# Performance work log

Measured on AMD Instinct MI355X. Metric: run time of the kernel, lower is better.

Reference implementation:

```python
import jax, jax.numpy as jnp
import numpy as np

N_EXPERTS = 16
IN_DIM = 1024
OUT_DIM = 1024
BATCH = 4096

def setup_inputs() -> dict:
    key = jax.random.key(0)
    k1, k2, k3, k4 = jax.random.split(key, 4)
    x = jax.random.normal(k1, (BATCH, IN_DIM), dtype=jnp.float32)
    comp_weight = jax.random.uniform(k2, (BATCH, N_EXPERTS), dtype=jnp.float32)
    # torch.rand init (uniform [0,1)) per original module
    weight = jax.random.uniform(k3, (N_EXPERTS, IN_DIM, OUT_DIM), dtype=jnp.float32)
    bias = jax.random.uniform(k4, (N_EXPERTS, OUT_DIM), dtype=jnp.float32)
    return {"x": x, "comp_weight": comp_weight, "weight": weight, "bias": bias}

def reference(x, comp_weight, weight, bias):
    # z[n,b,o] = x[b,i] @ weight[n,i,o] + bias[n,o]   (baddbmm)
    z = jnp.einsum('bi,nio->nbo', x, weight) + bias[:, None, :]
    # out[b,o] = sum_n comp_weight[b,n] * z[n,b,o]    (bmm combine)
    out = jnp.einsum('bn,nbo->bo', comp_weight, z)
    return jax.nn.relu(out)
```

## Files before the change

### kernel.cpp

```cpp
#include <hip/hip_runtime.h>
#include <hip/hip_bf16.h>
#include <cstdint>

#define BATCH   4096
#define IN_DIM  1024
#define OUT_DIM 1024
#define NEXP    16

typedef __bf16 bf16;
typedef __attribute__((ext_vector_type(8))) __bf16 bf16x8;
typedef __attribute__((ext_vector_type(4))) float  f32x4;

#define AS1 __attribute__((address_space(1)))
#define AS3 __attribute__((address_space(3)))

__device__ __forceinline__ void gld_lds16(const bf16* g, bf16* l) {
    __builtin_amdgcn_global_load_lds((const AS1 void*)g, (AS3 void*)l, 16, 0, 0);
}

__global__ __launch_bounds__(256) void convert_all(
        const float* __restrict__ x, const float* __restrict__ W,
        bf16* __restrict__ xt, bf16* __restrict__ wt) {
    __shared__ float Ls[64][65];
    int t = threadIdx.x;
    int bid = blockIdx.x;
    if (bid < 4096) {
        int nblk = bid >> 8, ne = (bid >> 4) & 15, ks = bid & 15;
        int kb = ne * 1024 + ks * 64;
        int n0 = nblk * 64;
#pragma unroll
        for (int r = 0; r < 4; r++) {
            int idx = r * 256 + t;
            int row = idx >> 4, c4 = (idx & 15) * 4;
            f32x4 v = *(const f32x4*)(W + (size_t)(kb + row) * OUT_DIM + n0 + c4);
#pragma unroll
            for (int j = 0; j < 4; j++) Ls[row][c4 + j] = v[j];
        }
        __syncthreads();
#pragma unroll
        for (int r = 0; r < 2; r++) {
            int c = r * 256 + t;
            int sub = c >> 6, l = c & 63;
            int lr = l & 15, lq = l >> 4;
            int kk = sub >> 2, wn = (sub >> 1) & 1, nt = sub & 1;
            int krow = kk * 32 + lq * 8;
            int col = wn * 32 + nt * 16 + lr;
            bf16x8 v;
#pragma unroll
            for (int j = 0; j < 8; j++) v[j] = (bf16)Ls[krow + j][col];
            *(bf16x8*)(wt + (size_t)bid * 4096 + c * 8) = v;
        }
    } else {
        int tile = bid - 4096;
        int mblk = tile >> 4, ks = tile & 15;
#pragma unroll
        for (int r = 0; r < 4; r++) {
            int q = r * 256 + t;
            int m_loc = q >> 3, sc = q & 7;
            int cc = sc ^ (m_loc & 7);
            const float* src = x + (size_t)(mblk * 128 + m_loc) * IN_DIM + ks * 64 + cc * 8;
            f32x4 a = *(const f32x4*)src;
            f32x4 b = *(const f32x4*)(src + 4);
            bf16x8 v;
#pragma unroll
            for (int j = 0; j < 4; j++) { v[j] = (bf16)a[j]; v[4 + j] = (bf16)b[j]; }
            *(bf16x8*)(xt + (size_t)tile * 8192 + q * 8) = v;
        }
    }
}

__global__ __launch_bounds__(512, 4) void moe_gemm(
        const float* __restrict__ cw, const float* __restrict__ bias,
        const bf16* __restrict__ xt, const bf16* __restrict__ wt,
        float* __restrict__ out) {
    int nblk = blockIdx.x;
    int mblk = blockIdx.y;
    int m0 = mblk * 128, n0 = nblk * 64;
    int t = threadIdx.x;
    int lane = t & 63, w = t >> 6;
    int wm = w >> 2, wn = w & 3;
    int lq = lane >> 4, lr = lane & 15;

    __shared__ bf16 As[128 * 64];
    __shared__ bf16 Bs[4][64 * 64];
    __shared__ float cwS[128][20];

    {
        f32x4 v = *(const f32x4*)(cw + (size_t)m0 * NEXP + t * 4);
        *(f32x4*)&cwS[t >> 2][(t & 3) * 4] = v;
    }

    const f32x4 fz = {0.f, 0.f, 0.f, 0.f};
    f32x4 acc[4];
#pragma unroll
    for (int mt = 0; mt < 4; mt++) acc[mt] = fz;

    int swz = lr & 7;
    int mrow[4];
#pragma unroll
    for (int mt = 0; mt < 4; mt++) mrow[mt] = (wm * 64 + mt * 16 + lr) * 64;

    const bf16* abase = xt + (size_t)(mblk * 16) * 8192;
    const bf16* bbase = wt + (size_t)nblk * (16 * 16 * 4096);

#pragma unroll 1
    for (int ks = 0; ks < 16; ks++) {
        const bf16* asrc = abase + (size_t)ks * 8192 + t * 8;
        gld_lds16(asrc,        &As[t * 8]);
        gld_lds16(asrc + 4096, &As[4096 + t * 8]);
        gld_lds16(bbase + (size_t)ks * 4096 + t * 8,        &Bs[0][t * 8]);
        gld_lds16(bbase + (size_t)(16 + ks) * 4096 + t * 8, &Bs[1][t * 8]);
        __syncthreads();

        bf16x8 af[4][2];
#pragma unroll
        for (int kk = 0; kk < 2; kk++)
#pragma unroll
            for (int mt = 0; mt < 4; mt++)
                af[mt][kk] = *(const bf16x8*)&As[mrow[mt] + ((kk * 4 + lq) ^ swz) * 8];

        f32x4 sg[4];
#pragma unroll
        for (int ne = 0; ne < 16; ne++) {
            if ((ne & 3) == 0) {
#pragma unroll
                for (int mt = 0; mt < 4; mt++)
                    sg[mt] = *(const f32x4*)&cwS[wm * 64 + mt * 16 + lr][ne];
            }
            if ((ne & 1) == 0 && ne < 14) {
                gld_lds16(bbase + (size_t)((ne + 2) * 16 + ks) * 4096 + t * 8,
                          &Bs[(ne + 2) & 3][t * 8]);
                gld_lds16(bbase + (size_t)((ne + 3) * 16 + ks) * 4096 + t * 8,
                          &Bs[(ne + 3) & 3][t * 8]);
            }
            bf16x8 bfr[2];
#pragma unroll
            for (int kk = 0; kk < 2; kk++)
                bfr[kk] = *(const bf16x8*)
                    &Bs[ne & 3][(kk * 4 + wn) * 512 + lane * 8];
#pragma unroll
            for (int mt = 0; mt < 4; mt++) {
                float sv = sg[mt][ne & 3];
                f32x4 p = __builtin_amdgcn_mfma_f32_16x16x32_bf16(
                    bfr[0], af[mt][0], fz, 0, 0, 0);
                p = __builtin_amdgcn_mfma_f32_16x16x32_bf16(
                    bfr[1], af[mt][1], p, 0, 0, 0);
                acc[mt] += sv * p;
            }
            if (ne & 1) __syncthreads();
        }
    }

    {
        bf16x8 acw[4];
#pragma unroll
        for (int mt = 0; mt < 4; mt++) {
            bf16x8 v;
#pragma unroll
            for (int j = 0; j < 8; j++) v[j] = (bf16)0.f;
            if (lq < 2) {
                int row = m0 + wm * 64 + mt * 16 + lr;
                f32x4 a = *(const f32x4*)(cw + (size_t)row * NEXP + lq * 8);
                f32x4 b = *(const f32x4*)(cw + (size_t)row * NEXP + lq * 8 + 4);
#pragma unroll
                for (int j = 0; j < 4; j++) { v[j] = (bf16)a[j]; v[4 + j] = (bf16)b[j]; }
            }
            acw[mt] = v;
        }
        bf16x8 bb;
        {
            bf16x8 v;
#pragma unroll
            for (int j = 0; j < 8; j++) v[j] = (bf16)0.f;
            if (lq < 2) {
                int col = n0 + wn * 16 + lr;
#pragma unroll
                for (int j = 0; j < 8; j++)
                    v[j] = (bf16)bias[(size_t)(lq * 8 + j) * OUT_DIM + col];
            }
            bb = v;
        }
#pragma unroll
        for (int mt = 0; mt < 4; mt++)
            acc[mt] = __builtin_amdgcn_mfma_f32_16x16x32_bf16(
                bb, acw[mt], acc[mt], 0, 0, 0);
    }

#pragma unroll
    for (int mt = 0; mt < 4; mt++) {
        int row = m0 + wm * 64 + mt * 16 + lr;
        int col = n0 + wn * 16 + lq * 4;
        f32x4 v = acc[mt];
#pragma unroll
        for (int r2 = 0; r2 < 4; r2++) v[r2] = v[r2] > 0.f ? v[r2] : 0.f;
        *(f32x4*)(out + (size_t)row * OUT_DIM + col) = v;
    }
}

__global__ void fallback_kernel(const float* __restrict__ x, const float* __restrict__ cw,
                                const float* __restrict__ W, const float* __restrict__ bias,
                                float* __restrict__ out) {
    int o = blockIdx.x * 256 + threadIdx.x;
    int b = o >> 10, oc = o & 1023;
    const float* xr = x + (size_t)b * IN_DIM;
    float accv = 0.f;
    for (int n = 0; n < NEXP; n++) {
        const float* wr = W + (size_t)n * IN_DIM * OUT_DIM + oc;
        float z = 0.f;
        for (int i = 0; i < IN_DIM; i++) z += xr[i] * wr[(size_t)i * OUT_DIM];
        accv += cw[(size_t)b * NEXP + n] * (z + bias[n * OUT_DIM + oc]);
    }
    out[o] = accv > 0.f ? accv : 0.f;
}

extern "C" void kernel_launch(void* const* d_in, const int* in_sizes, int n_in,
                              void* d_out, int out_size, void* d_ws, size_t ws_size,
                              hipStream_t stream) {
    const float* x    = (const float*)d_in[0];
    const float* cw   = (const float*)d_in[1];
    const float* W    = (const float*)d_in[2];
    const float* bias = (const float*)d_in[3];
    float* out = (float*)d_out;

    const size_t wt_elems = (size_t)NEXP * IN_DIM * OUT_DIM;
    const size_t xt_elems = (size_t)BATCH * IN_DIM;
    if (ws_size < (wt_elems + xt_elems) * sizeof(bf16)) {
        fallback_kernel<<<(BATCH * OUT_DIM) / 256, 256, 0, stream>>>(x, cw, W, bias, out);
        return;
    }
    bf16* wt = (bf16*)d_ws;
    bf16* xt = wt + wt_elems;

    convert_all<<<4096 + 512, 256, 0, stream>>>(x, W, xt, wt);
    moe_gemm<<<dim3(16, 32), 512, 0, stream>>>(cw, bias, xt, wt, out);
}
```

Baseline: 245.9 us.

## Double-buffer A and B tiles in LDS with 4-expert group prefetch

```diff
diff --git a/kernel.cpp b/kernel.cpp
--- a/kernel.cpp
+++ b/kernel.cpp
@@ -69,7 +69,7 @@
     }
 }
 
-__global__ __launch_bounds__(512, 4) void moe_gemm(
+__global__ __launch_bounds__(512, 2) void moe_gemm(
         const float* __restrict__ cw, const float* __restrict__ bias,
         const bf16* __restrict__ xt, const bf16* __restrict__ wt,
         float* __restrict__ out) {
@@ -81,8 +81,8 @@
     int wm = w >> 2, wn = w & 3;
     int lq = lane >> 4, lr = lane & 15;
 
-    __shared__ bf16 As[128 * 64];
-    __shared__ bf16 Bs[4][64 * 64];
+    __shared__ bf16 As[2][128 * 64];
+    __shared__ bf16 Bs[2][4][64 * 64];
     __shared__ float cwS[128][20];
 
     {
@@ -103,51 +103,66 @@
     const bf16* abase = xt + (size_t)(mblk * 16) * 8192;
     const bf16* bbase = wt + (size_t)nblk * (16 * 16 * 4096);
 
+    {
+        const bf16* a0 = abase + t * 8;
+        gld_lds16(a0,        &As[0][t * 8]);
+        gld_lds16(a0 + 4096, &As[0][4096 + t * 8]);
+#pragma unroll
+        for (int e = 0; e < 4; e++)
+            gld_lds16(bbase + (size_t)(e * 16) * 4096 + t * 8, &Bs[0][e][t * 8]);
+    }
+    __syncthreads();
+
+    bf16x8 af[4][2];
+    f32x4 sg[4];
+
 #pragma unroll 1
     for (int ks = 0; ks < 16; ks++) {
-        const bf16* asrc = abase + (size_t)ks * 8192 + t * 8;
-        gld_lds16(asrc,        &As[t * 8]);
-        gld_lds16(asrc + 4096, &As[4096 + t * 8]);
-        gld_lds16(bbase + (size_t)ks * 4096 + t * 8,        &Bs[0][t * 8]);
-        gld_lds16(bbase + (size_t)(16 + ks) * 4096 + t * 8, &Bs[1][t * 8]);
-        __syncthreads();
-
-        bf16x8 af[4][2];
-#pragma unroll
-        for (int kk = 0; kk < 2; kk++)
+#pragma unroll
+        for (int g = 0; g < 4; g++) {
+            if (g < 3) {
+#pragma unroll
+                for (int e = 0; e < 4; e++)
+                    gld_lds16(bbase + (size_t)(((g + 1) * 4 + e) * 16 + ks) * 4096 + t * 8,
+                              &Bs[(g + 1) & 1][e][t * 8]);
+            } else if (ks < 15) {
+#pragma unroll
+                for (int e = 0; e < 4; e++)
+                    gld_lds16(bbase + (size_t)(e * 16 + ks + 1) * 4096 + t * 8,
+                              &Bs[0][e][t * 8]);
+                const bf16* an = abase + (size_t)(ks + 1) * 8192 + t * 8;
+                gld_lds16(an,        &As[(ks + 1) & 1][t * 8]);
+                gld_lds16(an + 4096, &As[(ks + 1) & 1][4096 + t * 8]);
+            }
+            if (g == 0) {
+#pragma unroll
+                for (int kk = 0; kk < 2; kk++)
+#pragma unroll
+                    for (int mt = 0; mt < 4; mt++)
+                        af[mt][kk] = *(const bf16x8*)
+                            &As[ks & 1][mrow[mt] + ((kk * 4 + lq) ^ swz) * 8];
+            }
 #pragma unroll
             for (int mt = 0; mt < 4; mt++)
-                af[mt][kk] = *(const bf16x8*)&As[mrow[mt] + ((kk * 4 + lq) ^ swz) * 8];
-
-        f32x4 sg[4];
-#pragma unroll
-        for (int ne = 0; ne < 16; ne++) {
-            if ((ne & 3) == 0) {
-#pragma unroll
-                for (int mt = 0; mt < 4; mt++)
-                    sg[mt] = *(const f32x4*)&cwS[wm * 64 + mt * 16 + lr][ne];
-            }
-            if ((ne & 1) == 0 && ne < 14) {
-                gld_lds16(bbase + (size_t)((ne + 2) * 16 + ks) * 4096 + t * 8,
-                          &Bs[(ne + 2) & 3][t * 8]);
-                gld_lds16(bbase + (size_t)((ne + 3) * 16 + ks) * 4096 + t * 8,
-                          &Bs[(ne + 3) & 3][t * 8]);
-            }
-            bf16x8 bfr[2];
-#pragma unroll
-            for (int kk = 0; kk < 2; kk++)
-                bfr[kk] = *(const bf16x8*)
-                    &Bs[ne & 3][(kk * 4 + wn) * 512 + lane * 8];
-#pragma unroll
-            for (int mt = 0; mt < 4; mt++) {
-                float sv = sg[mt][ne & 3];
-                f32x4 p = __builtin_amdgcn_mfma_f32_16x16x32_bf16(
-                    bfr[0], af[mt][0], fz, 0, 0, 0);
-                p = __builtin_amdgcn_mfma_f32_16x16x32_bf16(
-                    bfr[1], af[mt][1], p, 0, 0, 0);
-                acc[mt] += sv * p;
-            }
-            if (ne & 1) __syncthreads();
+                sg[mt] = *(const f32x4*)&cwS[wm * 64 + mt * 16 + lr][g * 4];
+#pragma unroll
+            for (int e = 0; e < 4; e++) {
+                bf16x8 bfr[2];
+#pragma unroll
+                for (int kk = 0; kk < 2; kk++)
+                    bfr[kk] = *(const bf16x8*)
+                        &Bs[g & 1][e][(kk * 4 + wn) * 512 + lane * 8];
+#pragma unroll
+                for (int mt = 0; mt < 4; mt++) {
+                    float sv = sg[mt][e];
+                    f32x4 p = __builtin_amdgcn_mfma_f32_16x16x32_bf16(
+                        bfr[0], af[mt][0], fz, 0, 0, 0);
+                    p = __builtin_amdgcn_mfma_f32_16x16x32_bf16(
+                        bfr[1], af[mt][1], p, 0, 0, 0);
+                    acc[mt] += sv * p;
+                }
+            }
+            __syncthreads();
         }
     }
 
```

After: 431.4 us. 1.75x slower.

## Load GEMM operand fragments directly from global memory, dropping LDS staging

Applied to the files above, without the earlier changes.

```diff
diff --git a/kernel.cpp b/kernel.cpp
--- a/kernel.cpp
+++ b/kernel.cpp
@@ -13,10 +13,6 @@
 
 #define AS1 __attribute__((address_space(1)))
 #define AS3 __attribute__((address_space(3)))
-
-__device__ __forceinline__ void gld_lds16(const bf16* g, bf16* l) {
-    __builtin_amdgcn_global_load_lds((const AS1 void*)g, (AS3 void*)l, 16, 0, 0);
-}
 
 __global__ __launch_bounds__(256) void convert_all(
         const float* __restrict__ x, const float* __restrict__ W,
@@ -69,7 +65,7 @@
     }
 }
 
-__global__ __launch_bounds__(512, 4) void moe_gemm(
+__global__ __launch_bounds__(512, 2) void moe_gemm(
         const float* __restrict__ cw, const float* __restrict__ bias,
         const bf16* __restrict__ xt, const bf16* __restrict__ wt,
         float* __restrict__ out) {
@@ -81,14 +77,13 @@
     int wm = w >> 2, wn = w & 3;
     int lq = lane >> 4, lr = lane & 15;
 
-    __shared__ bf16 As[128 * 64];
-    __shared__ bf16 Bs[4][64 * 64];
     __shared__ float cwS[128][20];
 
     {
         f32x4 v = *(const f32x4*)(cw + (size_t)m0 * NEXP + t * 4);
         *(f32x4*)&cwS[t >> 2][(t & 3) * 4] = v;
     }
+    __syncthreads();
 
     const f32x4 fz = {0.f, 0.f, 0.f, 0.f};
     f32x4 acc[4];
@@ -101,53 +96,43 @@
     for (int mt = 0; mt < 4; mt++) mrow[mt] = (wm * 64 + mt * 16 + lr) * 64;
 
     const bf16* abase = xt + (size_t)(mblk * 16) * 8192;
-    const bf16* bbase = wt + (size_t)nblk * (16 * 16 * 4096);
+    const bf16* bbase = wt + (size_t)nblk * (16 * 16 * 4096) + lane * 8;
+    const float* cwrow0 = &cwS[wm * 64 + lr][0];
 
 #pragma unroll 1
     for (int ks = 0; ks < 16; ks++) {
-        const bf16* asrc = abase + (size_t)ks * 8192 + t * 8;
-        gld_lds16(asrc,        &As[t * 8]);
-        gld_lds16(asrc + 4096, &As[4096 + t * 8]);
-        gld_lds16(bbase + (size_t)ks * 4096 + t * 8,        &Bs[0][t * 8]);
-        gld_lds16(bbase + (size_t)(16 + ks) * 4096 + t * 8, &Bs[1][t * 8]);
-        __syncthreads();
-
         bf16x8 af[4][2];
+        const bf16* asrc = abase + (size_t)ks * 8192;
 #pragma unroll
         for (int kk = 0; kk < 2; kk++)
 #pragma unroll
             for (int mt = 0; mt < 4; mt++)
-                af[mt][kk] = *(const bf16x8*)&As[mrow[mt] + ((kk * 4 + lq) ^ swz) * 8];
-
-        f32x4 sg[4];
-#pragma unroll
-        for (int ne = 0; ne < 16; ne++) {
-            if ((ne & 3) == 0) {
-#pragma unroll
-                for (int mt = 0; mt < 4; mt++)
-                    sg[mt] = *(const f32x4*)&cwS[wm * 64 + mt * 16 + lr][ne];
+                af[mt][kk] = *(const bf16x8*)
+                    (asrc + mrow[mt] + ((kk * 4 + lq) ^ swz) * 8);
+
+#pragma unroll 1
+        for (int ne4 = 0; ne4 < 4; ne4++) {
+            f32x4 sg[4];
+#pragma unroll
+            for (int mt = 0; mt < 4; mt++)
+                sg[mt] = *(const f32x4*)(cwrow0 + mt * (16 * 20) + ne4 * 4);
+#pragma unroll
+            for (int e = 0; e < 4; e++) {
+                const bf16* btile = bbase + (size_t)((ne4 * 4 + e) * 16 + ks) * 4096;
+                bf16x8 bfr[2];
+#pragma unroll
+                for (int kk = 0; kk < 2; kk++)
+                    bfr[kk] = *(const bf16x8*)(btile + (kk * 4 + wn) * 512);
+#pragma unroll
+                for (int mt = 0; mt < 4; mt++) {
+                    float sv = sg[mt][e];
+                    f32x4 p = __builtin_amdgcn_mfma_f32_16x16x32_bf16(
+                        bfr[0], af[mt][0], fz, 0, 0, 0);
+                    p = __builtin_amdgcn_mfma_f32_16x16x32_bf16(
+                        bfr[1], af[mt][1], p, 0, 0, 0);
+                    acc[mt] += sv * p;
+                }
             }
-            if ((ne & 1) == 0 && ne < 14) {
-                gld_lds16(bbase + (size_t)((ne + 2) * 16 + ks) * 4096 + t * 8,
-                          &Bs[(ne + 2) & 3][t * 8]);
-                gld_lds16(bbase + (size_t)((ne + 3) * 16 + ks) * 4096 + t * 8,
-                          &Bs[(ne + 3) & 3][t * 8]);
-            }
-            bf16x8 bfr[2];
-#pragma unroll
-            for (int kk = 0; kk < 2; kk++)
-                bfr[kk] = *(const bf16x8*)
-                    &Bs[ne & 3][(kk * 4 + wn) * 512 + lane * 8];
-#pragma unroll
-            for (int mt = 0; mt < 4; mt++) {
-                float sv = sg[mt][ne & 3];
-                f32x4 p = __builtin_amdgcn_mfma_f32_16x16x32_bf16(
-                    bfr[0], af[mt][0], fz, 0, 0, 0);
-                p = __builtin_amdgcn_mfma_f32_16x16x32_bf16(
-                    bfr[1], af[mt][1], p, 0, 0, 0);
-                acc[mt] += sv * p;
-            }
-            if (ne & 1) __syncthreads();
         }
     }
 
```

Result: slower. 254.4 us (+3.5%).
